# Optimization experiments

Hardware: AMD Instinct MI355X
Metric: run time of the kernel (lower is better)

Reference implementation:

```python
import jax, jax.numpy as jnp
import numpy as np

B, S, D, UNITS = 32, 2048, 1024, 1024


def setup_inputs() -> dict:
    key = jax.random.key(0)
    ks = jax.random.split(key, 8)
    query = jax.random.normal(ks[0], (B, D), dtype=jnp.float32)
    values = jax.random.normal(ks[1], (B, S, D), dtype=jnp.float32)
    # Glorot-ish scaled params
    W1 = jax.random.normal(ks[2], (D, UNITS), dtype=jnp.float32) / np.sqrt(D)
    b1 = jnp.zeros((UNITS,), dtype=jnp.float32)
    W2 = jax.random.normal(ks[3], (D, UNITS), dtype=jnp.float32) / np.sqrt(D)
    b2 = jnp.zeros((UNITS,), dtype=jnp.float32)
    V = jax.random.normal(ks[4], (UNITS, 1), dtype=jnp.float32) / np.sqrt(UNITS)
    bv = jnp.zeros((1,), dtype=jnp.float32)
    return {"query": query, "values": values, "W1": W1, "b1": b1,
            "W2": W2, "b2": b2, "V": V, "bv": bv}


def reference(query, values, W1, b1, W2, b2, V, bv):
    # query: [B, D]; values: [B, S, D]
    kv = jnp.einsum("bsd,du->bsu", values, W1) + b1          # [B, S, U]
    q = (query @ W2 + b2)[:, None, :]                          # [B, 1, U]
    score = jnp.tanh(kv + q) @ V + bv                          # [B, S, 1]
    attention_weights = jax.nn.softmax(score, axis=1)          # [B, S, 1]
    context_vector = jnp.sum(attention_weights * values, axis=1)  # [B, D]
    return context_vector, attention_weights
```

## Files before the change

kernel.cpp:

```cpp
#include <hip/hip_runtime.h>
#include <hip/hip_bf16.h>

#define B_ 32
#define S_ 2048
#define D_ 1024
#define U_ 1024
#define M_ (B_ * S_)

typedef __attribute__((ext_vector_type(8))) short bf16x8;
typedef __attribute__((ext_vector_type(4))) float f32x4;

__device__ __forceinline__ unsigned short f2bf(float x) {
  unsigned int u = __float_as_uint(x);
  unsigned int r = (u + 0x7FFFu + ((u >> 16) & 1u)) >> 16;
  return (unsigned short)r;
}

__device__ __forceinline__ void gload_lds16(const void* g, void* l) {
  __builtin_amdgcn_global_load_lds(
      (const __attribute__((address_space(1))) unsigned int*)g,
      (__attribute__((address_space(3))) unsigned int*)l, 16, 0, 0);
}

__global__ void k_cvt(const float* __restrict__ v, unsigned short* __restrict__ o, int n8) {
  int i = blockIdx.x * blockDim.x + threadIdx.x;
  int stride = gridDim.x * blockDim.x;
  for (; i < n8; i += stride) {
    const float4* p = (const float4*)(v + (size_t)i * 8);
    float4 a = p[0];
    float4 b = p[1];
    uint4 r;
    r.x = (unsigned)f2bf(a.x) | ((unsigned)f2bf(a.y) << 16);
    r.y = (unsigned)f2bf(a.z) | ((unsigned)f2bf(a.w) << 16);
    r.z = (unsigned)f2bf(b.x) | ((unsigned)f2bf(b.y) << 16);
    r.w = (unsigned)f2bf(b.z) | ((unsigned)f2bf(b.w) << 16);
    ((uint4*)o)[i] = r;
  }
}

__global__ void k_transpose(const float* __restrict__ w1, unsigned short* __restrict__ w1t) {
  __shared__ float tile[32][33];
  int u0 = blockIdx.x * 32, d0 = blockIdx.y * 32;
  int tx = threadIdx.x & 31, ty = threadIdx.x >> 5;
  #pragma unroll
  for (int i = 0; i < 32; i += 8)
    tile[ty + i][tx] = w1[(size_t)(d0 + ty + i) * U_ + u0 + tx];
  __syncthreads();
  #pragma unroll
  for (int i = 0; i < 32; i += 8)
    w1t[(size_t)(u0 + ty + i) * D_ + d0 + tx] = f2bf(tile[tx][ty + i]);
}

__global__ void k_q(const float* __restrict__ query, const float* __restrict__ w2,
                    const float* __restrict__ b1, const float* __restrict__ b2,
                    float* __restrict__ q2) {
  int u = blockIdx.x * 256 + threadIdx.x;
  int b = blockIdx.y;
  const float* qr = query + b * D_;
  float acc = 0.f;
  #pragma unroll 8
  for (int d = 0; d < D_; ++d) acc = fmaf(qr[d], w2[(size_t)d * U_ + u], acc);
  q2[b * U_ + u] = acc + b1[u] + b2[u];
}

#define BM 128
#define BN 128
#define BK 64

__launch_bounds__(256, 2)
__global__ void k_gemm_score(const unsigned short* __restrict__ A,
                             const unsigned short* __restrict__ Bt,
                             const float* __restrict__ q2,
                             const float* __restrict__ V,
                             float* __restrict__ scores)
{
  __shared__ unsigned short As[BM * BK];
  __shared__ unsigned short Bs[BN * BK];
  const int tid = threadIdx.x, wid = tid >> 6, lane = tid & 63;
  const int bn = blockIdx.x, bm = blockIdx.y;
  const int row0 = bm * BM, col0 = bn * BN;
  const int b_idx = row0 / S_;

  const int srow = lane >> 3;
  const int skcol = (lane & 7) * 8;

  f32x4 acc[4][4];
  #pragma unroll
  for (int m = 0; m < 4; ++m)
    #pragma unroll
    for (int n = 0; n < 4; ++n) acc[m][n] = (f32x4){0.f, 0.f, 0.f, 0.f};

  const unsigned short* Ag = A + (size_t)row0 * D_;
  const unsigned short* Bg = Bt + (size_t)col0 * D_;
  const int am = (wid >> 1) * 64;
  const int an = (wid & 1) * 64;

  for (int kt = 0; kt < D_; kt += BK) {
    #pragma unroll
    for (int c = 0; c < 4; ++c) {
      const int r = wid * 4 + c;
      gload_lds16(Ag + (size_t)(r * 8 + srow) * D_ + kt + skcol, &As[r * 512]);
      gload_lds16(Bg + (size_t)(r * 8 + srow) * D_ + kt + skcol, &Bs[r * 512]);
    }
    __syncthreads();
    #pragma unroll
    for (int ks = 0; ks < 2; ++ks) {
      bf16x8 af[4], bfr[4];
      const int kf = ks * 32 + (lane >> 4) * 8;
      #pragma unroll
      for (int m = 0; m < 4; ++m)
        af[m] = *(const bf16x8*)&As[(am + m * 16 + (lane & 15)) * BK + kf];
      #pragma unroll
      for (int n = 0; n < 4; ++n)
        bfr[n] = *(const bf16x8*)&Bs[(an + n * 16 + (lane & 15)) * BK + kf];
      #pragma unroll
      for (int m = 0; m < 4; ++m)
        #pragma unroll
        for (int n = 0; n < 4; ++n)
          acc[m][n] = __builtin_amdgcn_mfma_f32_16x16x32_bf16(af[m], bfr[n], acc[m][n], 0, 0, 0);
    }
    __syncthreads();
  }

  const int colb = lane & 15, rowg = lane >> 4;
  #pragma unroll
  for (int m = 0; m < 4; ++m) {
    float s0 = 0.f, s1 = 0.f, s2 = 0.f, s3 = 0.f;
    #pragma unroll
    for (int n = 0; n < 4; ++n) {
      const int u = col0 + an + n * 16 + colb;
      const float qv = q2[b_idx * U_ + u];
      const float vv = V[u];
      s0 += tanhf(acc[m][n][0] + qv) * vv;
      s1 += tanhf(acc[m][n][1] + qv) * vv;
      s2 += tanhf(acc[m][n][2] + qv) * vv;
      s3 += tanhf(acc[m][n][3] + qv) * vv;
    }
    #pragma unroll
    for (int off = 1; off < 16; off <<= 1) {
      s0 += __shfl_xor(s0, off);
      s1 += __shfl_xor(s1, off);
      s2 += __shfl_xor(s2, off);
      s3 += __shfl_xor(s3, off);
    }
    if (colb == 0) {
      const int r = row0 + am + m * 16 + rowg * 4;
      atomicAdd(&scores[r + 0], s0);
      atomicAdd(&scores[r + 1], s1);
      atomicAdd(&scores[r + 2], s2);
      atomicAdd(&scores[r + 3], s3);
    }
  }
}

__global__ void k_softmax(const float* __restrict__ scores, float* __restrict__ attw) {
  const int b = blockIdx.x;
  const float* s = scores + b * S_;
  const int tid = threadIdx.x;
  __shared__ float wred[4], wsum[4];
  float v[8];
  float lmax = -1e30f;
  #pragma unroll
  for (int i = 0; i < 8; ++i) {
    v[i] = s[tid + i * 256];
    lmax = fmaxf(lmax, v[i]);
  }
  #pragma unroll
  for (int off = 32; off > 0; off >>= 1) lmax = fmaxf(lmax, __shfl_xor(lmax, off));
  if ((tid & 63) == 0) wred[tid >> 6] = lmax;
  __syncthreads();
  const float bmax = fmaxf(fmaxf(wred[0], wred[1]), fmaxf(wred[2], wred[3]));
  float lsum = 0.f;
  #pragma unroll
  for (int i = 0; i < 8; ++i) {
    v[i] = expf(v[i] - bmax);
    lsum += v[i];
  }
  #pragma unroll
  for (int off = 32; off > 0; off >>= 1) lsum += __shfl_xor(lsum, off);
  if ((tid & 63) == 0) wsum[tid >> 6] = lsum;
  __syncthreads();
  const float inv = 1.f / (wsum[0] + wsum[1] + wsum[2] + wsum[3]);
  #pragma unroll
  for (int i = 0; i < 8; ++i) attw[b * S_ + tid + i * 256] = v[i] * inv;
}

__global__ void k_context(const float* __restrict__ values, const float* __restrict__ attw,
                          float* __restrict__ ctx) {
  const int b = blockIdx.y;
  const int s0 = blockIdx.x * (S_ / 16);
  const int t = threadIdx.x;
  const float* vb = values + (size_t)b * S_ * D_;
  float4 acc = make_float4(0.f, 0.f, 0.f, 0.f);
  for (int s = s0; s < s0 + S_ / 16; ++s) {
    const float w = attw[b * S_ + s];
    const float4 v = *(const float4*)(vb + (size_t)s * D_ + t * 4);
    acc.x = fmaf(w, v.x, acc.x);
    acc.y = fmaf(w, v.y, acc.y);
    acc.z = fmaf(w, v.z, acc.z);
    acc.w = fmaf(w, v.w, acc.w);
  }
  float* c = ctx + b * D_ + t * 4;
  atomicAdd(c + 0, acc.x);
  atomicAdd(c + 1, acc.y);
  atomicAdd(c + 2, acc.z);
  atomicAdd(c + 3, acc.w);
}

extern "C" void kernel_launch(void* const* d_in, const int* in_sizes, int n_in,
                              void* d_out, int out_size, void* d_ws, size_t ws_size,
                              hipStream_t stream) {
  const float* query = (const float*)d_in[0];
  const float* values = (const float*)d_in[1];
  const float* W1 = (const float*)d_in[2];
  const float* b1 = (const float*)d_in[3];
  const float* W2 = (const float*)d_in[4];
  const float* b2 = (const float*)d_in[5];
  const float* V = (const float*)d_in[6];

  float* out = (float*)d_out;
  float* ctx = out;
  float* attw = out + B_ * D_;

  char* ws = (char*)d_ws;
  const size_t VBF_BYTES = (size_t)M_ * D_ * 2;
  const size_t W1T_BYTES = (size_t)U_ * D_ * 2;
  const size_t Q2_BYTES = (size_t)B_ * U_ * 4;
  unsigned short* vbf = (unsigned short*)ws;
  unsigned short* w1t = (unsigned short*)(ws + VBF_BYTES);
  float* q2 = (float*)(ws + VBF_BYTES + W1T_BYTES);
  float* scores = (float*)(ws + VBF_BYTES + W1T_BYTES + Q2_BYTES);

  hipMemsetAsync(scores, 0, (size_t)M_ * 4, stream);
  hipMemsetAsync(ctx, 0, (size_t)B_ * D_ * 4, stream);

  k_cvt<<<2048, 256, 0, stream>>>(values, vbf, M_ * D_ / 8);
  k_transpose<<<dim3(U_ / 32, D_ / 32), 256, 0, stream>>>(W1, w1t);
  k_q<<<dim3(U_ / 256, B_), 256, 0, stream>>>(query, W2, b1, b2, q2);
  k_gemm_score<<<dim3(U_ / BN, M_ / BM), 256, 0, stream>>>(vbf, w1t, q2, V, scores);
  k_softmax<<<B_, 256, 0, stream>>>(scores, attw);
  k_context<<<dim3(16, B_), 256, 0, stream>>>(values, attw, ctx);
}
```

Before: 720.6 us.

## Use fast tanh, swizzle GEMM tile order, split-K the query projection

Three separate changes. The score epilogue swaps tanhf for an exp2/rcp-based tanh approximation, which cuts transcendental cost at some accuracy risk. The GEMM block index is remapped so groups of 8 M-tiles run across all N-tiles together, aiming for better L2 reuse of the A rows. The query-projection kernel is split over 8 D-chunks with a shared-memory reduction, so it launches many more blocks and gets more parallelism.

```diff
diff --git a/kernel.cpp b/kernel.cpp
--- a/kernel.cpp
+++ b/kernel.cpp
@@ -14,6 +14,11 @@
   unsigned int u = __float_as_uint(x);
   unsigned int r = (u + 0x7FFFu + ((u >> 16) & 1u)) >> 16;
   return (unsigned short)r;
+}
+
+__device__ __forceinline__ float fast_tanh(float x) {
+  float e = __builtin_amdgcn_exp2f(x * 2.88539008177793f);
+  return 1.0f - 2.0f * __builtin_amdgcn_rcpf(e + 1.0f);
 }
 
 __device__ __forceinline__ void gload_lds16(const void* g, void* l) {
@@ -54,13 +59,22 @@
 __global__ void k_q(const float* __restrict__ query, const float* __restrict__ w2,
                     const float* __restrict__ b1, const float* __restrict__ b2,
                     float* __restrict__ q2) {
-  int u = blockIdx.x * 256 + threadIdx.x;
-  int b = blockIdx.y;
+  const int ul = threadIdx.x & 31, dg = threadIdx.x >> 5;
+  const int u = blockIdx.x * 32 + ul;
+  const int b = blockIdx.y;
   const float* qr = query + b * D_;
   float acc = 0.f;
+  const int d0 = dg * 128;
   #pragma unroll 8
-  for (int d = 0; d < D_; ++d) acc = fmaf(qr[d], w2[(size_t)d * U_ + u], acc);
-  q2[b * U_ + u] = acc + b1[u] + b2[u];
+  for (int d = d0; d < d0 + 128; ++d) acc = fmaf(qr[d], w2[(size_t)d * U_ + u], acc);
+  __shared__ float red[8][32];
+  red[dg][ul] = acc;
+  __syncthreads();
+  if (dg == 0) {
+    float s = red[0][ul] + red[1][ul] + red[2][ul] + red[3][ul] +
+              red[4][ul] + red[5][ul] + red[6][ul] + red[7][ul];
+    q2[b * U_ + u] = s + b1[u] + b2[u];
+  }
 }
 
 #define BM 128
@@ -77,7 +91,10 @@
   __shared__ unsigned short As[BM * BK];
   __shared__ unsigned short Bs[BN * BK];
   const int tid = threadIdx.x, wid = tid >> 6, lane = tid & 63;
-  const int bn = blockIdx.x, bm = blockIdx.y;
+
+  const int L = blockIdx.x + blockIdx.y * 8;
+  const int bn = (L >> 3) & 7;
+  const int bm = (L & 7) + ((L >> 6) << 3);
   const int row0 = bm * BM, col0 = bn * BN;
   const int b_idx = row0 / S_;
 
@@ -131,10 +148,10 @@
       const int u = col0 + an + n * 16 + colb;
       const float qv = q2[b_idx * U_ + u];
       const float vv = V[u];
-      s0 += tanhf(acc[m][n][0] + qv) * vv;
-      s1 += tanhf(acc[m][n][1] + qv) * vv;
-      s2 += tanhf(acc[m][n][2] + qv) * vv;
-      s3 += tanhf(acc[m][n][3] + qv) * vv;
+      s0 += fast_tanh(acc[m][n][0] + qv) * vv;
+      s1 += fast_tanh(acc[m][n][1] + qv) * vv;
+      s2 += fast_tanh(acc[m][n][2] + qv) * vv;
+      s3 += fast_tanh(acc[m][n][3] + qv) * vv;
     }
     #pragma unroll
     for (int off = 1; off < 16; off <<= 1) {
@@ -236,7 +253,7 @@
 
   k_cvt<<<2048, 256, 0, stream>>>(values, vbf, M_ * D_ / 8);
   k_transpose<<<dim3(U_ / 32, D_ / 32), 256, 0, stream>>>(W1, w1t);
-  k_q<<<dim3(U_ / 256, B_), 256, 0, stream>>>(query, W2, b1, b2, q2);
+  k_q<<<dim3(U_ / 32, B_), 256, 0, stream>>>(query, W2, b1, b2, q2);
   k_gemm_score<<<dim3(U_ / BN, M_ / BM), 256, 0, stream>>>(vbf, w1t, q2, V, scores);
   k_softmax<<<B_, 256, 0, stream>>>(scores, attw);
   k_context<<<dim3(16, B_), 256, 0, stream>>>(values, attw, ctx);
```

Result: faster. 642.8 us (-10.8%).
